# Kernel optimization log

Hardware: AMD Instinct MI355X
Metric: run time of the kernel (lower is better)

The kernel has to match this reference:

```python
import jax, jax.numpy as jnp
import numpy as np

N, C, D, H, W = 4, 64, 64, 64, 64
MIP = 8  # max(8, 64 // 32)
BN_EPS = 1e-5


def _hardswish(x):
    return x * jnp.clip(x + 3.0, 0.0, 6.0) * (1.0 / 6.0)


def setup_inputs() -> dict:
    key = jax.random.key(0)
    ks = jax.random.split(key, 8)
    s = lambda k, shape: jax.random.normal(k, shape, jnp.float32) * 0.05
    return {
        "x": jax.random.normal(ks[0], (N, C, D, H, W), jnp.float32),
        "conv1_w": s(ks[1], (MIP, C)),   # 1x1x1 conv == channel matmul
        "conv1_b": s(ks[2], (MIP,)),
        "bn_gamma": jnp.ones((MIP,), jnp.float32),
        "bn_beta": jnp.zeros((MIP,), jnp.float32),
        "bn_mean": jnp.zeros((MIP,), jnp.float32),
        "bn_var": jnp.ones((MIP,), jnp.float32),
        "convd_w": s(ks[3], (C, MIP)),
        "convd_b": s(ks[4], (C,)),
        "convh_w": s(ks[5], (C, MIP)),
        "convh_b": s(ks[6], (C,)),
        "convw_w": s(ks[7], (C, MIP)),
        "convw_b": jnp.zeros((C,), jnp.float32),
    }


def reference(x, conv1_w, conv1_b, bn_gamma, bn_beta, bn_mean, bn_var,
              convd_w, convd_b, convh_w, convh_b, convw_w, convw_b):
    n, c, d, h, w = x.shape
    # Three 1-axis-preserving adaptive avg pools -> [n, c, axis_len]
    xd = x.mean(axis=(3, 4))  # keep D
    xh = x.mean(axis=(2, 4))  # keep H
    xw = x.mean(axis=(2, 3))  # keep W
    y = jnp.concatenate([xd, xh, xw], axis=2)  # [n, c, d+h+w]
    # shared 1x1 conv + BN(eval) + Hardswish
    y = jnp.einsum('ncl,mc->nml', y, conv1_w) + conv1_b[None, :, None]
    scale = bn_gamma / jnp.sqrt(bn_var + BN_EPS)
    y = (y - bn_mean[None, :, None]) * scale[None, :, None] + bn_beta[None, :, None]
    y = _hardswish(y)
    yd, yh, yw = y[:, :, :d], y[:, :, d:d + h], y[:, :, d + h:]
    ad = jax.nn.sigmoid(jnp.einsum('nml,om->nol', yd, convd_w) + convd_b[None, :, None])
    ah = jax.nn.sigmoid(jnp.einsum('nml,om->nol', yh, convh_w) + convh_b[None, :, None])
    aw = jax.nn.sigmoid(jnp.einsum('nml,om->nol', yw, convw_w) + convw_b[None, :, None])
    # triple broadcast multiply: [n,c,d,1,1] * [n,c,1,h,1] * [n,c,1,1,w]
    return x * ad[:, :, :, None, None] * ah[:, :, None, :, None] * aw[:, :, None, None, :]
```

## Files before the change

kernel.cpp:

```cpp
#include <hip/hip_runtime.h>

typedef unsigned int uint;
typedef unsigned short ushort;
typedef float __attribute__((ext_vector_type(4))) f32x4;

__global__ __launch_bounds__(1024) void pool_k(const float* __restrict__ x,
                                               float* __restrict__ pool) {
    const int blk = blockIdx.x;
    const int t = threadIdx.x;
    __shared__ float sd[64], sh[64], sw[64];
    if (t < 64) { sd[t] = 0.f; sh[t] = 0.f; sw[t] = 0.f; }
    __syncthreads();

    const int w4 = t & 15;
    const int h  = t >> 4;
    const float4* __restrict__ xp = (const float4*)(x + (size_t)blk * 262144);

    float accw[4] = {0,0,0,0};
    float acch = 0.f;

    #pragma unroll 4
    for (int d = 0; d < 64; ++d) {
        float4 v = xp[d * 1024 + t];
        accw[0] += v.x; accw[1] += v.y; accw[2] += v.z; accw[3] += v.w;
        float s = (v.x + v.y) + (v.z + v.w);
        acch += s;
        float r = s;
        r += __shfl_down(r, 32);
        r += __shfl_down(r, 16);
        r += __shfl_down(r, 8);
        r += __shfl_down(r, 4);
        r += __shfl_down(r, 2);
        r += __shfl_down(r, 1);
        if ((t & 63) == 0) atomicAdd(&sd[d], r);
    }
    atomicAdd(&sh[h], acch);
    #pragma unroll
    for (int j = 0; j < 4; ++j) atomicAdd(&sw[w4 * 4 + j], accw[j]);
    __syncthreads();

    if (t < 192) {
        float v = (t < 64) ? sd[t] : (t < 128) ? sh[t - 64] : sw[t - 128];
        const int n = blk >> 6, c = blk & 63;
        pool[(n * 192 + t) * 64 + c] = v * (1.0f / 4096.0f);
    }
}

__global__ __launch_bounds__(1024) void att_k(
    const float* __restrict__ x, const float* __restrict__ pool,
    const float* __restrict__ w1, const float* __restrict__ b1,
    const float* __restrict__ gam, const float* __restrict__ bet,
    const float* __restrict__ mu,  const float* __restrict__ var,
    const float* __restrict__ wd,  const float* __restrict__ bd,
    const float* __restrict__ wh,  const float* __restrict__ bh,
    const float* __restrict__ ww,  const float* __restrict__ bw,
    float* __restrict__ out)
{
    const int blk = blockIdx.x;
    const int n = blk >> 6, c = blk & 63;
    const int t = threadIdx.x;
    __shared__ float y_s[8][192];
    __shared__ float a_s[192];

    if (t < 192) {
        float acc[8] = {0,0,0,0,0,0,0,0};
        const float4* __restrict__ pp = (const float4*)(pool + (n * 192 + t) * 64);
        #pragma unroll 4
        for (int c4 = 0; c4 < 16; ++c4) {
            float4 p = pp[c4];
            const int cb = c4 * 4;
            #pragma unroll
            for (int m = 0; m < 8; ++m) {
                acc[m] += p.x * w1[m * 64 + cb]
                        + p.y * w1[m * 64 + cb + 1]
                        + p.z * w1[m * 64 + cb + 2]
                        + p.w * w1[m * 64 + cb + 3];
            }
        }
        #pragma unroll
        for (int m = 0; m < 8; ++m) {
            float scale = gam[m] * rsqrtf(var[m] + 1e-5f);
            float v = (acc[m] + b1[m] - mu[m]) * scale + bet[m];
            float hs = v * fminf(fmaxf(v + 3.0f, 0.0f), 6.0f) * (1.0f / 6.0f);
            y_s[m][t] = hs;
        }
    }
    __syncthreads();

    if (t < 192) {
        const float* wsel; float bsel;
        if (t < 64)       { wsel = wd + c * 8; bsel = bd[c]; }
        else if (t < 128) { wsel = wh + c * 8; bsel = bh[c]; }
        else              { wsel = ww + c * 8; bsel = bw[c]; }
        float v = bsel;
        #pragma unroll
        for (int m = 0; m < 8; ++m) v += y_s[m][t] * wsel[m];
        a_s[t] = 1.0f / (1.0f + __expf(-v));
    }
    __syncthreads();

    const int w4 = t & 15;
    const int h  = t >> 4;
    f32x4 gw;
    gw.x = a_s[128 + w4 * 4 + 0];
    gw.y = a_s[128 + w4 * 4 + 1];
    gw.z = a_s[128 + w4 * 4 + 2];
    gw.w = a_s[128 + w4 * 4 + 3];
    const float ahr = a_s[64 + h];
    const f32x4* __restrict__ xp = (const f32x4*)(x   + (size_t)blk * 262144);
    f32x4*       __restrict__ op = (f32x4*)      (out + (size_t)blk * 262144);

    #pragma unroll 2
    for (int k = 0; k < 64; ++k) {
        const int g = t + (k << 10);
        const float s = a_s[k] * ahr;
        f32x4 v = xp[g];
        f32x4 o = v * (gw * s);
        __builtin_nontemporal_store(o, &op[g]);
    }
}

extern "C" void kernel_launch(void* const* d_in, const int* in_sizes, int n_in,
                              void* d_out, int out_size, void* d_ws, size_t ws_size,
                              hipStream_t stream) {
    const float* x = (const float*)d_in[0];
    float* pool = (float*)d_ws;

    pool_k<<<256, 1024, 0, stream>>>(x, pool);
    att_k<<<256, 1024, 0, stream>>>(x, pool,
        (const float*)d_in[1],  (const float*)d_in[2],
        (const float*)d_in[3],  (const float*)d_in[4],
        (const float*)d_in[5],  (const float*)d_in[6],
        (const float*)d_in[7],  (const float*)d_in[8],
        (const float*)d_in[9],  (const float*)d_in[10],
        (const float*)d_in[11], (const float*)d_in[12],
        (float*)d_out);
}
```

Measured before the change: 510.6 us.

## Fuse pooling and attention kernels via cooperative grid sync with register/LDS stash

Merges the pooling kernel and the attention-apply kernel into one cooperative kernel separated by a grid-wide barrier. The first 19 depth slices of each block's x slab are kept in registers (16) and LDS (3), so the second pass re-reads fewer bytes from global memory. The remaining slices are reloaded with nontemporal loads. The change trades a kernel launch and part of the x re-read for a grid sync and heavy register/LDS pressure, which may limit occupancy. It also depends on all 256 blocks being co-resident.

```diff
diff --git a/kernel.cpp b/kernel.cpp
--- a/kernel.cpp
+++ b/kernel.cpp
@@ -1,27 +1,43 @@
 #include <hip/hip_runtime.h>
+#include <hip/hip_cooperative_groups.h>
 
-typedef unsigned int uint;
-typedef unsigned short ushort;
+namespace cg = cooperative_groups;
+
 typedef float __attribute__((ext_vector_type(4))) f32x4;
 
-__global__ __launch_bounds__(1024) void pool_k(const float* __restrict__ x,
-                                               float* __restrict__ pool) {
+#define RSTASH 16
+#define LSTASH 3
+
+__global__ __launch_bounds__(1024, 4) void coord_att_k(
+    const float* __restrict__ x,
+    const float* __restrict__ w1, const float* __restrict__ b1,
+    const float* __restrict__ gam, const float* __restrict__ bet,
+    const float* __restrict__ mu,  const float* __restrict__ var,
+    const float* __restrict__ wd,  const float* __restrict__ bd,
+    const float* __restrict__ wh,  const float* __restrict__ bh,
+    const float* __restrict__ ww,  const float* __restrict__ bw,
+    float* __restrict__ out, float* __restrict__ pool)
+{
     const int blk = blockIdx.x;
-    const int t = threadIdx.x;
+    const int n = blk >> 6, c = blk & 63;
+    const int t  = threadIdx.x;
+    const int w4 = t & 15;
+    const int h  = t >> 4;
+
     __shared__ float sd[64], sh[64], sw[64];
+    __shared__ float a_s[192];
+    __shared__ f32x4 stash[LSTASH * 1024];
+
     if (t < 64) { sd[t] = 0.f; sh[t] = 0.f; sw[t] = 0.f; }
     __syncthreads();
 
-    const int w4 = t & 15;
-    const int h  = t >> 4;
-    const float4* __restrict__ xp = (const float4*)(x + (size_t)blk * 262144);
+    const f32x4* __restrict__ xp = (const f32x4*)(x + (size_t)blk * 262144);
 
+    f32x4 xr[RSTASH];
     float accw[4] = {0,0,0,0};
     float acch = 0.f;
 
-    #pragma unroll 4
-    for (int d = 0; d < 64; ++d) {
-        float4 v = xp[d * 1024 + t];
+    auto proc = [&](f32x4 v, int d) {
         accw[0] += v.x; accw[1] += v.y; accw[2] += v.z; accw[3] += v.w;
         float s = (v.x + v.y) + (v.z + v.w);
         acch += s;
@@ -33,6 +49,24 @@
         r += __shfl_down(r, 2);
         r += __shfl_down(r, 1);
         if ((t & 63) == 0) atomicAdd(&sd[d], r);
+    };
+
+    #pragma unroll
+    for (int d = 0; d < RSTASH; ++d) {
+        f32x4 v = xp[d * 1024 + t];
+        xr[d] = v;
+        proc(v, d);
+    }
+    #pragma unroll
+    for (int d = RSTASH; d < RSTASH + LSTASH; ++d) {
+        f32x4 v = xp[d * 1024 + t];
+        stash[(d - RSTASH) * 1024 + t] = v;
+        proc(v, d);
+    }
+    #pragma unroll 4
+    for (int d = RSTASH + LSTASH; d < 64; ++d) {
+        f32x4 v = xp[d * 1024 + t];
+        proc(v, d);
     }
     atomicAdd(&sh[h], acch);
     #pragma unroll
@@ -41,33 +75,18 @@
 
     if (t < 192) {
         float v = (t < 64) ? sd[t] : (t < 128) ? sh[t - 64] : sw[t - 128];
-        const int n = blk >> 6, c = blk & 63;
         pool[(n * 192 + t) * 64 + c] = v * (1.0f / 4096.0f);
     }
-}
 
-__global__ __launch_bounds__(1024) void att_k(
-    const float* __restrict__ x, const float* __restrict__ pool,
-    const float* __restrict__ w1, const float* __restrict__ b1,
-    const float* __restrict__ gam, const float* __restrict__ bet,
-    const float* __restrict__ mu,  const float* __restrict__ var,
-    const float* __restrict__ wd,  const float* __restrict__ bd,
-    const float* __restrict__ wh,  const float* __restrict__ bh,
-    const float* __restrict__ ww,  const float* __restrict__ bw,
-    float* __restrict__ out)
-{
-    const int blk = blockIdx.x;
-    const int n = blk >> 6, c = blk & 63;
-    const int t = threadIdx.x;
-    __shared__ float y_s[8][192];
-    __shared__ float a_s[192];
+    __threadfence();
+    cg::this_grid().sync();
 
     if (t < 192) {
         float acc[8] = {0,0,0,0,0,0,0,0};
-        const float4* __restrict__ pp = (const float4*)(pool + (n * 192 + t) * 64);
+        const f32x4* __restrict__ pp = (const f32x4*)(pool + (n * 192 + t) * 64);
         #pragma unroll 4
         for (int c4 = 0; c4 < 16; ++c4) {
-            float4 p = pp[c4];
+            f32x4 p = pp[c4];
             const int cb = c4 * 4;
             #pragma unroll
             for (int m = 0; m < 8; ++m) {
@@ -77,62 +96,77 @@
                         + p.w * w1[m * 64 + cb + 3];
             }
         }
-        #pragma unroll
-        for (int m = 0; m < 8; ++m) {
-            float scale = gam[m] * rsqrtf(var[m] + 1e-5f);
-            float v = (acc[m] + b1[m] - mu[m]) * scale + bet[m];
-            float hs = v * fminf(fmaxf(v + 3.0f, 0.0f), 6.0f) * (1.0f / 6.0f);
-            y_s[m][t] = hs;
-        }
-    }
-    __syncthreads();
-
-    if (t < 192) {
         const float* wsel; float bsel;
         if (t < 64)       { wsel = wd + c * 8; bsel = bd[c]; }
         else if (t < 128) { wsel = wh + c * 8; bsel = bh[c]; }
         else              { wsel = ww + c * 8; bsel = bw[c]; }
-        float v = bsel;
+        float vg = bsel;
         #pragma unroll
-        for (int m = 0; m < 8; ++m) v += y_s[m][t] * wsel[m];
-        a_s[t] = 1.0f / (1.0f + __expf(-v));
+        for (int m = 0; m < 8; ++m) {
+            float scale = gam[m] * rsqrtf(var[m] + 1e-5f);
+            float yv = (acc[m] + b1[m] - mu[m]) * scale + bet[m];
+            float hs = yv * fminf(fmaxf(yv + 3.0f, 0.0f), 6.0f) * (1.0f / 6.0f);
+            vg += hs * wsel[m];
+        }
+        a_s[t] = 1.0f / (1.0f + __expf(-vg));
     }
     __syncthreads();
 
-    const int w4 = t & 15;
-    const int h  = t >> 4;
     f32x4 gw;
     gw.x = a_s[128 + w4 * 4 + 0];
     gw.y = a_s[128 + w4 * 4 + 1];
     gw.z = a_s[128 + w4 * 4 + 2];
     gw.w = a_s[128 + w4 * 4 + 3];
     const float ahr = a_s[64 + h];
-    const f32x4* __restrict__ xp = (const f32x4*)(x   + (size_t)blk * 262144);
-    f32x4*       __restrict__ op = (f32x4*)      (out + (size_t)blk * 262144);
+    f32x4* __restrict__ op = (f32x4*)(out + (size_t)blk * 262144);
 
+    #pragma unroll
+    for (int k = 0; k < RSTASH; ++k) {
+        const float s = a_s[k] * ahr;
+        f32x4 o = xr[k] * (gw * s);
+        __builtin_nontemporal_store(o, &op[k * 1024 + t]);
+    }
+    #pragma unroll
+    for (int k = RSTASH; k < RSTASH + LSTASH; ++k) {
+        const float s = a_s[k] * ahr;
+        f32x4 o = stash[(k - RSTASH) * 1024 + t] * (gw * s);
+        __builtin_nontemporal_store(o, &op[k * 1024 + t]);
+    }
     #pragma unroll 2
-    for (int k = 0; k < 64; ++k) {
-        const int g = t + (k << 10);
+    for (int k = RSTASH + LSTASH; k < 64; ++k) {
         const float s = a_s[k] * ahr;
-        f32x4 v = xp[g];
+        f32x4 v = __builtin_nontemporal_load(&xp[k * 1024 + t]);
         f32x4 o = v * (gw * s);
-        __builtin_nontemporal_store(o, &op[g]);
+        __builtin_nontemporal_store(o, &op[k * 1024 + t]);
     }
 }
 
 extern "C" void kernel_launch(void* const* d_in, const int* in_sizes, int n_in,
                               void* d_out, int out_size, void* d_ws, size_t ws_size,
                               hipStream_t stream) {
-    const float* x = (const float*)d_in[0];
+    const float* x   = (const float*)d_in[0];
+    const float* w1  = (const float*)d_in[1];
+    const float* b1  = (const float*)d_in[2];
+    const float* gam = (const float*)d_in[3];
+    const float* bet = (const float*)d_in[4];
+    const float* mu  = (const float*)d_in[5];
+    const float* var = (const float*)d_in[6];
+    const float* wd  = (const float*)d_in[7];
+    const float* bd  = (const float*)d_in[8];
+    const float* wh  = (const float*)d_in[9];
+    const float* bh  = (const float*)d_in[10];
+    const float* ww  = (const float*)d_in[11];
+    const float* bw  = (const float*)d_in[12];
+    float* out  = (float*)d_out;
     float* pool = (float*)d_ws;
 
-    pool_k<<<256, 1024, 0, stream>>>(x, pool);
-    att_k<<<256, 1024, 0, stream>>>(x, pool,
-        (const float*)d_in[1],  (const float*)d_in[2],
-        (const float*)d_in[3],  (const float*)d_in[4],
-        (const float*)d_in[5],  (const float*)d_in[6],
-        (const float*)d_in[7],  (const float*)d_in[8],
-        (const float*)d_in[9],  (const float*)d_in[10],
-        (const float*)d_in[11], (const float*)d_in[12],
-        (float*)d_out);
+    void* args[] = {
+        (void*)&x,
+        (void*)&w1, (void*)&b1, (void*)&gam, (void*)&bet,
+        (void*)&mu, (void*)&var, (void*)&wd, (void*)&bd,
+        (void*)&wh, (void*)&bh, (void*)&ww, (void*)&bw,
+        (void*)&out, (void*)&pool
+    };
+    hipLaunchCooperativeKernel((const void*)coord_att_k,
+                               dim3(256), dim3(1024), args, 0, stream);
 }
```

Result: slower. 741.2 us (+45.2%).

## Split each (n,c) volume across four 256-thread blocks with global atomic pooling

Applied to the files above, without the earlier changes.

Both kernels now use 1024 blocks of 256 threads instead of 256 blocks of 1024, with each block handling a 16-slice quarter of D for one (n,c). Partial H and W pool sums are combined with global atomics, so a zeroing kernel is added beforehand. The attention kernel recomputes the shared MLP in every quarter-block (4x redundant) and uses nontemporal loads for x. The intent is more blocks for better occupancy and load balance across CUs, at the cost of an extra launch, global atomics and duplicated small MLP work.

```diff
diff --git a/kernel.cpp b/kernel.cpp
--- a/kernel.cpp
+++ b/kernel.cpp
@@ -1,52 +1,82 @@
 #include <hip/hip_runtime.h>
 
-typedef unsigned int uint;
-typedef unsigned short ushort;
 typedef float __attribute__((ext_vector_type(4))) f32x4;
 
-__global__ __launch_bounds__(1024) void pool_k(const float* __restrict__ x,
-                                               float* __restrict__ pool) {
-    const int blk = blockIdx.x;
+
+__global__ __launch_bounds__(1024) void zero_k(float* __restrict__ p) {
+    p[blockIdx.x * 1024 + threadIdx.x] = 0.f;
+}
+
+__global__ __launch_bounds__(256) void pool_k(const float* __restrict__ x,
+                                              float* __restrict__ pool) {
+    const int b   = blockIdx.x;
+    const int blk = b >> 2;
+    const int q   = b & 3;
+    const int n = blk >> 6, c = blk & 63;
+    const int d0 = q * 16;
     const int t = threadIdx.x;
-    __shared__ float sd[64], sh[64], sw[64];
-    if (t < 64) { sd[t] = 0.f; sh[t] = 0.f; sw[t] = 0.f; }
+    const int w = t >> 6, l = t & 63;
+
+    __shared__ float sdp[16];
+    __shared__ float swp[64];
+    if (t < 16) sdp[t] = 0.f;
+    if (t < 64) swp[t] = 0.f;
     __syncthreads();
 
-    const int w4 = t & 15;
-    const int h  = t >> 4;
-    const float4* __restrict__ xp = (const float4*)(x + (size_t)blk * 262144);
+    const f32x4* __restrict__ xp = (const f32x4*)(x + (size_t)blk * 262144);
 
     float accw[4] = {0,0,0,0};
-    float acch = 0.f;
+    float acch[4] = {0,0,0,0};
 
-    #pragma unroll 4
-    for (int d = 0; d < 64; ++d) {
-        float4 v = xp[d * 1024 + t];
-        accw[0] += v.x; accw[1] += v.y; accw[2] += v.z; accw[3] += v.w;
-        float s = (v.x + v.y) + (v.z + v.w);
-        acch += s;
-        float r = s;
+    for (int dd = 0; dd < 16; ++dd) {
+        float sacc = 0.f;
+        #pragma unroll
+        for (int i = 0; i < 4; ++i) {
+            f32x4 v = xp[(d0 + dd) * 1024 + i * 256 + t];
+            accw[0] += v.x; accw[1] += v.y; accw[2] += v.z; accw[3] += v.w;
+            float s = (v.x + v.y) + (v.z + v.w);
+            sacc += s;
+            acch[i] += s;
+        }
+        float r = sacc;
         r += __shfl_down(r, 32);
         r += __shfl_down(r, 16);
         r += __shfl_down(r, 8);
         r += __shfl_down(r, 4);
         r += __shfl_down(r, 2);
         r += __shfl_down(r, 1);
-        if ((t & 63) == 0) atomicAdd(&sd[d], r);
+        if (l == 0) atomicAdd(&sdp[dd], r);
     }
-    atomicAdd(&sh[h], acch);
+
     #pragma unroll
-    for (int j = 0; j < 4; ++j) atomicAdd(&sw[w4 * 4 + j], accw[j]);
+    for (int i = 0; i < 4; ++i) {
+        float r = acch[i];
+        r += __shfl_xor(r, 1);
+        r += __shfl_xor(r, 2);
+        r += __shfl_xor(r, 4);
+        r += __shfl_xor(r, 8);
+        if ((l & 15) == 0) {
+            const int h = i * 16 + w * 4 + (l >> 4);
+            atomicAdd(&pool[(n * 192 + 64 + h) * 64 + c], r * (1.0f / 4096.0f));
+        }
+    }
+
+    #pragma unroll
+    for (int j = 0; j < 4; ++j) {
+        float r = accw[j];
+        r += __shfl_down(r, 32);
+        r += __shfl_down(r, 16);
+        if (l < 16) atomicAdd(&swp[l * 4 + j], r);
+    }
     __syncthreads();
 
-    if (t < 192) {
-        float v = (t < 64) ? sd[t] : (t < 128) ? sh[t - 64] : sw[t - 128];
-        const int n = blk >> 6, c = blk & 63;
-        pool[(n * 192 + t) * 64 + c] = v * (1.0f / 4096.0f);
-    }
+    if (t < 16)
+        pool[(n * 192 + d0 + t) * 64 + c] = sdp[t] * (1.0f / 4096.0f);
+    if (t < 64)
+        atomicAdd(&pool[(n * 192 + 128 + t) * 64 + c], swp[t] * (1.0f / 4096.0f));
 }
 
-__global__ __launch_bounds__(1024) void att_k(
+__global__ __launch_bounds__(256) void att_k(
     const float* __restrict__ x, const float* __restrict__ pool,
     const float* __restrict__ w1, const float* __restrict__ b1,
     const float* __restrict__ gam, const float* __restrict__ bet,
@@ -56,18 +86,21 @@
     const float* __restrict__ ww,  const float* __restrict__ bw,
     float* __restrict__ out)
 {
-    const int blk = blockIdx.x;
+    const int b   = blockIdx.x;
+    const int blk = b >> 2;
+    const int q   = b & 3;
     const int n = blk >> 6, c = blk & 63;
+    const int d0 = q * 16;
     const int t = threadIdx.x;
     __shared__ float y_s[8][192];
     __shared__ float a_s[192];
 
     if (t < 192) {
         float acc[8] = {0,0,0,0,0,0,0,0};
-        const float4* __restrict__ pp = (const float4*)(pool + (n * 192 + t) * 64);
+        const f32x4* __restrict__ pp = (const f32x4*)(pool + (n * 192 + t) * 64);
         #pragma unroll 4
         for (int c4 = 0; c4 < 16; ++c4) {
-            float4 p = pp[c4];
+            f32x4 p = pp[c4];
             const int cb = c4 * 4;
             #pragma unroll
             for (int m = 0; m < 8; ++m) {
@@ -100,23 +133,28 @@
     __syncthreads();
 
     const int w4 = t & 15;
-    const int h  = t >> 4;
+    const int h4 = t >> 4;
     f32x4 gw;
     gw.x = a_s[128 + w4 * 4 + 0];
     gw.y = a_s[128 + w4 * 4 + 1];
     gw.z = a_s[128 + w4 * 4 + 2];
     gw.w = a_s[128 + w4 * 4 + 3];
-    const float ahr = a_s[64 + h];
+    float ahr[4];
+    #pragma unroll
+    for (int i = 0; i < 4; ++i) ahr[i] = a_s[64 + i * 16 + h4];
+
     const f32x4* __restrict__ xp = (const f32x4*)(x   + (size_t)blk * 262144);
     f32x4*       __restrict__ op = (f32x4*)      (out + (size_t)blk * 262144);
 
-    #pragma unroll 2
-    for (int k = 0; k < 64; ++k) {
-        const int g = t + (k << 10);
-        const float s = a_s[k] * ahr;
-        f32x4 v = xp[g];
-        f32x4 o = v * (gw * s);
-        __builtin_nontemporal_store(o, &op[g]);
+    #pragma unroll
+    for (int i = 0; i < 4; ++i) {
+        #pragma unroll 2
+        for (int dd = 0; dd < 16; ++dd) {
+            const int off = (d0 + dd) * 1024 + i * 256 + t;
+            const float s = a_s[d0 + dd] * ahr[i];
+            f32x4 v = __builtin_nontemporal_load(&xp[off]);
+            __builtin_nontemporal_store(v * (gw * s), &op[off]);
+        }
     }
 }
 
@@ -126,8 +164,9 @@
     const float* x = (const float*)d_in[0];
     float* pool = (float*)d_ws;
 
-    pool_k<<<256, 1024, 0, stream>>>(x, pool);
-    att_k<<<256, 1024, 0, stream>>>(x, pool,
+    zero_k<<<48, 1024, 0, stream>>>(pool);
+    pool_k<<<1024, 256, 0, stream>>>(x, pool);
+    att_k<<<1024, 256, 0, stream>>>(x, pool,
         (const float*)d_in[1],  (const float*)d_in[2],
         (const float*)d_in[3],  (const float*)d_in[4],
         (const float*)d_in[5],  (const float*)d_in[6],
```

After: 533.1 us. 4.4% more time.
